# Optimization experiments

Measured on AMD Instinct MI355X. Metric: run time of the kernel, lower is better.

The kernel has to match this reference:

```python
import jax, jax.numpy as jnp
import numpy as np

N = 10000      # nodes
E = 160000     # edges
F = 64         # channels (hidden_irreps 0e multiplicity)
NS = 10        # species
NB = 8         # num_bessel
NL = 4         # max_ell + 1
LM = 16        # total SH components (l=0..3)
RMAX = 10.0
AVG = 16.0     # avg_num_neighbors
L_OF = jnp.array([0,1,1,1,2,2,2,2,2,3,3,3,3,3,3,3])  # l index of each SH component


def _sph(u):
    """Component-normalized real spherical harmonics l=0..3 on unit vectors [E,3] -> [E,16]."""
    x, y, z = u[..., 0], u[..., 1], u[..., 2]
    s3, s5, s7 = 3.0**0.5, 5.0**0.5, 7.0**0.5
    s15, s42, s70, s105 = 15.0**0.5, 42.0**0.5, 70.0**0.5, 105.0**0.5
    one = jnp.ones_like(x)
    return jnp.stack([
        one,
        s3*x, s3*y, s3*z,
        s15*x*y, s15*y*z, (s5/2)*(3*z*z - 1), s15*x*z, (s15/2)*(x*x - y*y),
        (s70/4)*y*(3*x*x - y*y), s105*x*y*z, (s42/4)*y*(5*z*z - 1),
        (s7/2)*z*(5*z*z - 3), (s42/4)*x*(5*z*z - 1),
        (s105/2)*z*(x*x - y*y), (s70/4)*x*(x*x - 3*y*y),
    ], axis=-1)


def _bessel(r):
    """Bessel radial basis with smooth polynomial cutoff. r [E] -> [E,NB]."""
    n = jnp.arange(1, NB + 1, dtype=r.dtype)
    eb = (2.0 / RMAX) ** 0.5 * jnp.sin(n * jnp.pi * r[:, None] / RMAX) / (r[:, None] + 1e-9)
    p = 5.0
    xr = r / RMAX
    env = (1.0 - ((p+1)*(p+2)/2) * xr**p + p*(p+2) * xr**(p+1) - (p*(p+1)/2) * xr**(p+2))
    env = jnp.where(xr < 1.0, env, 0.0)
    return eb * env[:, None]


def _interaction(node_feats, node_attrs, Y, bess, senders, receivers,
                 W_up, Wr1, Wr2, Wr3, W_mix, W_sc, w_prod, last):
    # linear down-projection of scalar channel feeding the edge tensor product
    h = node_feats[:, :, 0] @ W_up                                   # [N,F]
    # per-edge radial weights, one per (channel, l) path
    R = jax.nn.silu(bess @ Wr1)
    R = jax.nn.silu(R @ Wr2)
    R = (R @ Wr3).reshape(E, F, NL)                                  # [E,F,4]
    Rlm = R[:, :, L_OF]                                              # [E,F,16]
    # edge tensor-product message: gather senders, modulate by radial, outer with SH
    m = h[senders][:, :, None] * Rlm * Y[:, None, :]                 # [E,F,16]
    A = jax.ops.segment_sum(m, receivers, num_segments=N) / AVG      # [N,F,16]
    # per-l channel mixing (equivariant linear)
    A = jnp.einsum('nfk,kfg->ngk', A, W_mix[L_OF])                   # [N,F,16]
    # species-dependent residual (skip tensor product with node attrs)
    wsp = jnp.einsum('ns,sfg->nfg', node_attrs, W_sc)                # [N,F,F]
    sc = jnp.einsum('nfk,nfg->ngk', node_feats, wsp)                 # [N,F,16]
    # symmetric product basis (correlation=3): scalar-modulated polynomial, equivariant
    s = A[:, :, 0]
    B = A * (w_prod[0] + w_prod[1]*s + w_prod[2]*s*s)[:, :, None]
    out = B + sc
    if last:  # last layer keeps only 0e (scalar) irreps
        out = out * (jnp.arange(LM) == 0).astype(out.dtype)
    return out


def _forward(positions, node_attrs, shifts, senders, receivers, w_embed,
             u0_up, u0_r1, u0_r2, u0_r3, u0_mix, u0_sc, u0_prod, w_read0,
             u1_up, u1_r1, u1_r2, u1_r3, u1_mix, u1_sc, u1_prod, w_mlp1, w_mlp2):
    vec = positions[receivers] - positions[senders] + shifts         # [E,3]
    r = jnp.linalg.norm(vec, axis=-1)
    Y = _sph(vec / (r[:, None] + 1e-9))                              # [E,16]
    bess = _bessel(r)                                                # [E,8]
    # node embedding into scalar channel of [N,F,16] state
    nf = jnp.zeros((N, F, LM), positions.dtype).at[:, :, 0].set(node_attrs @ w_embed)
    nf = _interaction(nf, node_attrs, Y, bess, senders, receivers,
                      u0_up, u0_r1, u0_r2, u0_r3, u0_mix, u0_sc, u0_prod, last=False)
    out0 = nf[:, :, 0] @ w_read0                                     # [N,1] linear readout
    nf = _interaction(nf, node_attrs, Y, bess, senders, receivers,
                      u1_up, u1_r1, u1_r2, u1_r3, u1_mix, u1_sc, u1_prod, last=True)
    out1 = jax.nn.silu(nf[:, :, 0] @ w_mlp1) @ w_mlp2                # [N,1] nonlinear readout
    return jnp.stack([out0, out1], axis=1)                           # [N,2,1]


def setup_inputs() -> dict:
    key = jax.random.key(0)
    ks = jax.random.split(key, 24)
    positions = jax.random.uniform(ks[0], (N, 3), jnp.float32) * 5.0
    species = jax.random.randint(ks[1], (N,), 0, NS)
    node_attrs = jax.nn.one_hot(species, NS, dtype=jnp.float32)
    shifts = jnp.zeros((E, 3), jnp.float32)
    senders = jax.random.randint(ks[2], (E,), 0, N, dtype=jnp.int32)
    receivers = jax.random.randint(ks[3], (E,), 0, N, dtype=jnp.int32)

    def nrm(k, shape, fan_in):
        return jax.random.normal(k, shape, jnp.float32) / (fan_in ** 0.5)

    d = dict(positions=positions, node_attrs=node_attrs, shifts=shifts,
             senders=senders, receivers=receivers,
             w_embed=nrm(ks[4], (NS, F), NS))
    for i, base in ((0, 5), (1, 13)):
        d[f'u{i}_up'] = nrm(ks[base], (F, F), F)
        d[f'u{i}_r1'] = nrm(ks[base+1], (NB, 64), NB)
        d[f'u{i}_r2'] = nrm(ks[base+2], (64, 64), 64)
        d[f'u{i}_r3'] = nrm(ks[base+3], (64, F*NL), 64)
        d[f'u{i}_mix'] = nrm(ks[base+4], (NL, F, F), F)
        d[f'u{i}_sc'] = nrm(ks[base+5], (NS, F, F), F)
        d[f'u{i}_prod'] = nrm(ks[base+6], (3, F), 1)
    d['w_read0'] = nrm(ks[12], (F, 1), F)
    d['w_mlp1'] = nrm(ks[20], (F, 16), F)
    d['w_mlp2'] = nrm(ks[21], (16, 1), 16)
    return d


def reference(positions, node_attrs, shifts, senders, receivers, w_embed,
              u0_up, u0_r1, u0_r2, u0_r3, u0_mix, u0_sc, u0_prod, w_read0,
              u1_up, u1_r1, u1_r2, u1_r3, u1_mix, u1_sc, u1_prod, w_mlp1, w_mlp2):
    return _forward(positions, node_attrs, shifts, senders, receivers, w_embed,
                    u0_up, u0_r1, u0_r2, u0_r3, u0_mix, u0_sc, u0_prod, w_read0,
                    u1_up, u1_r1, u1_r2, u1_r3, u1_mix, u1_sc, u1_prod, w_mlp1, w_mlp2)
```

## Files before the change

kernel.cpp:

```cpp
#include <hip/hip_runtime.h>
#include <hip/hip_bf16.h>
#include <cstdint>
#include <cstddef>

#define NN 10000
#define NE 160000

typedef unsigned short u16;
typedef __attribute__((ext_vector_type(8))) short short8;
typedef __attribute__((ext_vector_type(4))) float f32x4;

__device__ __forceinline__ float b2f(u16 u){
    union { uint32_t i; float f; } v; v.i = ((uint32_t)u) << 16; return v.f;
}
__device__ __forceinline__ u16 f2b(float f){
    union { __hip_bfloat16 h; u16 u; } c; c.h = __float2bfloat16(f); return c.u;
}
__device__ __forceinline__ u16 f2b_rne(float f){
    uint32_t b = __float_as_uint(f);
    return (u16)((b + 0x7FFFu + ((b >> 16) & 1u)) >> 16);
}
__device__ __forceinline__ float silu_f(float x){ return x / (1.f + __expf(-x)); }
__device__ __forceinline__ float ldr(const void* p, int i, int bf){
    return bf ? b2f(((const u16*)p)[i]) : ((const float*)p)[i];
}

constexpr size_t W_FLAG = 0;
constexpr size_t W_CNT  = 16;
constexpr size_t W_OFFS = 10016;
constexpr size_t W_SSND = 30032;
constexpr size_t W_ATT  = 350032;
constexpr size_t W_WGT  = 960032;
constexpr size_t OW_EMB = 0;
constexpr size_t OW_UP0 = 640;
constexpr size_t OW_R10 = 4736;
constexpr size_t OW_R20 = 5248;
constexpr size_t OW_R30 = 9344;
constexpr size_t OW_MIX0= 25728;
constexpr size_t OW_SC0 = 42112;
constexpr size_t OW_PR0 = 83072;
constexpr size_t OW_UP1 = 83264;
constexpr size_t OW_R11 = 87360;
constexpr size_t OW_R21 = 87872;
constexpr size_t OW_R31 = 91968;
constexpr size_t OW_MIX1= 108352;
constexpr size_t OW_SC1 = 124736;
constexpr size_t OW_PR1 = 165696;
constexpr size_t OW_RD0 = 165888;
constexpr size_t OW_ML1 = 165952;
constexpr size_t OW_ML2 = 166976;
constexpr size_t OW_TEND = 167000;
constexpr size_t W_BES  = W_WGT + OW_TEND;
constexpr size_t W_NF0  = W_BES + (size_t)NE*8;
constexpr size_t W_H    = W_NF0 + (size_t)NN*64;
constexpr size_t W_A    = W_H   + (size_t)NN*64;
constexpr size_t W_NF1  = W_A   + (size_t)NN*64;
constexpr size_t W_R0   = W_NF1 + (size_t)NN*64;
constexpr size_t W_R1   = W_R0  + (size_t)NE*32;
constexpr size_t WP_DUAL   = W_R1 + (size_t)NE*32;
constexpr size_t WP_SINGLE = W_R0 + (size_t)NE*32;
constexpr size_t W_RS_F = W_R0;
constexpr size_t WP_F   = W_R0 + NE;

constexpr size_t NEED_DUAL   = (WP_DUAL   + 10400) * 4;
constexpr size_t NEED_SINGLE = (WP_SINGLE + 10400) * 4;

constexpr int OCT  = 520;
constexpr int OCTS = 136;

__global__ void k_dh(const uint32_t* __restrict__ attrs, const int* __restrict__ rcv,
                     int* __restrict__ flag, int* __restrict__ cnt, int* __restrict__ rank){
    int i = blockIdx.x * 256 + threadIdx.x;
    int c = 0;
    if (i < 50000){
        uint32_t v = attrs[i];
        c = (v != 0u && v != 0x3F800000u) ? 1 : 0;
    }
    unsigned long long m = __ballot(c);
    if ((threadIdx.x & 63) == 0 && m)
        atomicAdd(flag, (int)__popcll(m));
    if (i < NE) rank[i] = atomicAdd(&cnt[rcv[i]], 1);
}

struct PrepArgs { const void* s[21]; float* d[21]; int n[21]; };
__global__ __launch_bounds__(1024) void k_scan_prep(PrepArgs a, const int* __restrict__ flag,
        const int* __restrict__ cnt, int* __restrict__ offs,
        u16* __restrict__ WP, float* __restrict__ nf0, float* __restrict__ h){
    int bf = flag[0] > 100;
    int t = threadIdx.x;
    if (blockIdx.x == 0){
        __shared__ int cl[10000];
        __shared__ int part[1024];
        for (int i = t; i < 10000; i += 1024) cl[i] = cnt[i];
        __syncthreads();
        int base = t * 10;
        int s = 0;
        #pragma unroll
        for (int i = 0; i < 10; i++) if (base + i < NN) s += cl[base + i];
        part[t] = s; __syncthreads();
        for (int d = 1; d < 1024; d <<= 1){
            int v = part[t];
            if (t >= d) v += part[t - d];
            __syncthreads();
            part[t] = v;
            __syncthreads();
        }
        int run = part[t] - s;
        #pragma unroll
        for (int i = 0; i < 10; i++){
            int idx = base + i;
            if (idx < NN){ offs[idx] = run; run += cl[idx]; }
        }
        if (t == 1023) offs[NN] = part[1023];
    } else if (blockIdx.x < 65){
        int stride = 64 * 1024;
        int t0 = (blockIdx.x - 1) * 1024 + t;
        for (int k = 0; k < 21; k++){
            float* d = a.d[k]; int n4 = a.n[k] >> 2;
            if (bf){
                const uint2* s = (const uint2*)a.s[k];
                for (int i = t0; i < n4; i += stride){
                    uint2 v = s[i];
                    float4 o;
                    o.x = b2f((u16)(v.x & 0xffffu));
                    o.y = b2f((u16)(v.x >> 16));
                    o.z = b2f((u16)(v.y & 0xffffu));
                    o.w = b2f((u16)(v.y >> 16));
                    ((float4*)d)[i] = o;
                }
            } else {
                const float4* s = (const float4*)a.s[k];
                for (int i = t0; i < n4; i += stride) ((float4*)d)[i] = s[i];
            }
        }
    } else if (blockIdx.x < 67){
        int b = blockIdx.x - 65;
        const void* W1 = a.s[b ? 12 : 5];
        const void* W2 = a.s[b ? 13 : 6];
        const void* W3 = a.s[b ? 14 : 7];
        u16* dst = WP + b * 10400;
        for (int i = t; i < 5200; i += 1024) ((uint32_t*)dst)[i] = 0;
        __syncthreads();
        for (int i = t; i < 512; i += 1024){
            int n = i >> 3, k = i & 7;
            dst[n*8 + k] = f2b(ldr(W1, k*64 + n, bf));
        }
        for (int i = t; i < 2048; i += 1024){
            int k = (i >> 6) * 2, n = i & 63;
            uint32_t p2 = ((uint32_t)f2b(ldr(W2, (k+1)*64 + n, bf)) << 16) | f2b(ldr(W2, k*64 + n, bf));
            uint32_t p3 = ((uint32_t)f2b(ldr(W3, (k+1)*256 + 4*n, bf)) << 16) | f2b(ldr(W3, k*256 + 4*n, bf));
            *(uint32_t*)&dst[2080 + (k>>3)*OCT + n*8 + (k&7)] = p2;
            *(uint32_t*)&dst[6240 + (k>>3)*OCT + n*8 + (k&7)] = p3;
        }
    } else {
        int nb = blockIdx.x - 67;
        int n = nb*16 + (t >> 6);
        int l = t & 63;
        const void* attrs = a.s[1];
        const void* Wemb  = a.s[3];
        const void* Wup0  = a.s[4];
        float acc = 0.f;
        #pragma unroll
        for (int s = 0; s < 10; s++) acc += ldr(attrs, n*10 + s, bf) * ldr(Wemb, s*64 + l, bf);
        nf0[n*64 + l] = acc;
        float hv = 0.f;
        #pragma unroll 16
        for (int g = 0; g < 64; g++) hv += __shfl(acc, g) * ldr(Wup0, g*64 + l, bf);
        h[n*64 + l] = hv;
    }
}

__global__ void k_scatter_r(const int* __restrict__ rcv, const int* __restrict__ snd,
        const void* __restrict__ posr, const void* __restrict__ shfr,
        const int* __restrict__ offs, const int* __restrict__ rank,
        int* __restrict__ ssnd, float* __restrict__ rs,
        const int* __restrict__ flag){
    int e = blockIdx.x * 256 + threadIdx.x;
    if (e >= NE) return;
    int bf = flag[0] > 100;
    int r = rcv[e], s = snd[e];
    float vx = ldr(posr, r*3+0, bf) - ldr(posr, s*3+0, bf) + ldr(shfr, e*3+0, bf);
    float vy = ldr(posr, r*3+1, bf) - ldr(posr, s*3+1, bf) + ldr(shfr, e*3+1, bf);
    float vz = ldr(posr, r*3+2, bf) - ldr(posr, s*3+2, bf) + ldr(shfr, e*3+2, bf);
    float rr = sqrtf(vx*vx + vy*vy + vz*vz);
    int p = offs[r] + rank[e];
    ssnd[p] = s;
    rs[p] = rr;
}

__global__ void k_bess(const float* __restrict__ rs, float* __restrict__ bessp){
    int p = blockIdx.x * 256 + threadIdx.x;
    if (p >= NE) return;
    float rr = rs[p];
    float xr = rr * 0.1f;
    float x2 = xr*xr; float x5 = x2*x2*xr;
    float env = 1.f - 21.f*x5 + 35.f*x5*xr - 15.f*x5*x2;
    if (xr >= 1.f) env = 0.f;
    float scl = 0.4472135954999579f * env / (rr + 1e-9f);
    float b[8];
    #pragma unroll
    for (int n = 1; n <= 8; n++)
        b[n-1] = scl * sinf((float)n * 3.14159265358979323846f * rr * 0.1f);
    float4* be = (float4*)(bessp + (size_t)p*8);
    be[0] = make_float4(b[0], b[1], b[2], b[3]);
    be[1] = make_float4(b[4], b[5], b[6], b[7]);
}

__global__ __launch_bounds__(256) void k_mlp_mfma(
        const int* __restrict__ rcv, const int* __restrict__ snd,
        const void* __restrict__ posr, const void* __restrict__ shfr,
        const int* __restrict__ offs, const int* __restrict__ rank,
        const u16* __restrict__ WPa, const u16* __restrict__ WPb,
        int* __restrict__ ssnd, u16* __restrict__ R0, u16* __restrict__ R1,
        int nblk0, const int* __restrict__ flag){
    __shared__ __align__(16) u16 W[10400];
    __shared__ __align__(16) u16 X[4][12*OCTS];
    int bf = flag[0] > 100;
    int half = blockIdx.x >= nblk0;
    int blk  = half ? blockIdx.x - nblk0 : blockIdx.x;
    const u16* WP = half ? WPb : WPa;
    u16* R = half ? R1 : R0;
    int t = threadIdx.x;
    int w = t >> 6, lane = t & 63;
    int q = lane >> 4, r = lane & 15;
    u16* Xw = &X[w][0];
    for (int i = t; i < 1300; i += 256) ((uint4*)W)[i] = ((const uint4*)WP)[i];
    int ge = blk*256 + w*64 + lane;
    int rn = rcv[ge], sn = snd[ge];
    int pv = offs[rn] + rank[ge];
    float vx = ldr(posr, rn*3+0, bf) - ldr(posr, sn*3+0, bf) + ldr(shfr, ge*3+0, bf);
    float vy = ldr(posr, rn*3+1, bf) - ldr(posr, sn*3+1, bf) + ldr(shfr, ge*3+1, bf);
    float vz = ldr(posr, rn*3+2, bf) - ldr(posr, sn*3+2, bf) + ldr(shfr, ge*3+2, bf);
    float rre = sqrtf(vx*vx + vy*vy + vz*vz);
    if (!half) ssnd[pv] = sn;
    {
        uint32_t* xz = (uint32_t*)(Xw + OCTS);
        for (int i = lane; i < 204; i += 64) xz[i] = 0;
    }
    __syncthreads();
    #pragma unroll 1
    for (int st = 0; st < 4; st++){
        int p0 = __shfl(pv, st*16 + q*4 + 0);
        int p1 = __shfl(pv, st*16 + q*4 + 1);
        int p2 = __shfl(pv, st*16 + q*4 + 2);
        int p3 = __shfl(pv, st*16 + q*4 + 3);
        {
            float rr = __shfl(rre, st*16 + (lane >> 2));
            float xr = rr * 0.1f;
            float x2 = xr*xr, x5 = x2*x2*xr;
            float env = 1.f - 21.f*x5 + 35.f*x5*xr - 15.f*x5*x2;
            if (xr >= 1.f) env = 0.f;
            float scl = 0.4472135954999579f * env / (rr + 1e-9f);
            int k0 = (lane & 3) * 2;
            float b0 = scl * __sinf((float)(k0+1) * 0.3141592653589793f * rr);
            float b1 = scl * __sinf((float)(k0+2) * 0.3141592653589793f * rr);
            ((uint32_t*)Xw)[lane] = ((uint32_t)f2b_rne(b1) << 16) | f2b_rne(b0);
        }
        {
            short8 a = *(const short8*)&Xw[q*OCTS + r*8];
            #pragma unroll
            for (int nt = 0; nt < 4; nt++){
                short8 b = *(const short8*)&W[q*OCT + (nt*16 + r)*8];
                f32x4 c = {0.f, 0.f, 0.f, 0.f};
                c = __builtin_amdgcn_mfma_f32_16x16x32_bf16(a, b, c, 0, 0, 0);
                #pragma unroll
                for (int g = 0; g < 4; g++){
                    int e = q*4 + g;
                    int n = nt*16 + r;
                    Xw[(4 + (n>>3))*OCTS + e*8 + (n&7)] = f2b_rne(silu_f(c[g]));
                }
            }
        }
        {
            short8 a0 = *(const short8*)&Xw[(4+q)*OCTS + r*8];
            short8 a1 = *(const short8*)&Xw[(8+q)*OCTS + r*8];
            #pragma unroll
            for (int nt = 0; nt < 4; nt++){
                short8 b0 = *(const short8*)&W[2080 + q*OCT + (nt*16 + r)*8];
                short8 b1 = *(const short8*)&W[2080 + (4+q)*OCT + (nt*16 + r)*8];
                f32x4 c = {0.f, 0.f, 0.f, 0.f};
                c = __builtin_amdgcn_mfma_f32_16x16x32_bf16(a0, b0, c, 0, 0, 0);
                c = __builtin_amdgcn_mfma_f32_16x16x32_bf16(a1, b1, c, 0, 0, 0);
                #pragma unroll
                for (int g = 0; g < 4; g++){
                    int e = q*4 + g;
                    int n = nt*16 + r;
                    Xw[(4 + (n>>3))*OCTS + e*8 + (n&7)] = f2b_rne(silu_f(c[g]));
                }
            }
        }
        {
            short8 a0 = *(const short8*)&Xw[(4+q)*OCTS + r*8];
            short8 a1 = *(const short8*)&Xw[(8+q)*OCTS + r*8];
            #pragma unroll
            for (int nt = 0; nt < 4; nt++){
                short8 b0 = *(const short8*)&W[6240 + q*OCT + (nt*16 + r)*8];
                short8 b1 = *(const short8*)&W[6240 + (4+q)*OCT + (nt*16 + r)*8];
                f32x4 c = {0.f, 0.f, 0.f, 0.f};
                c = __builtin_amdgcn_mfma_f32_16x16x32_bf16(a0, b0, c, 0, 0, 0);
                c = __builtin_amdgcn_mfma_f32_16x16x32_bf16(a1, b1, c, 0, 0, 0);
                int n = nt*16 + r;
                R[(size_t)p0*64 + n] = f2b_rne(c[0]);
                R[(size_t)p1*64 + n] = f2b_rne(c[1]);
                R[(size_t)p2*64 + n] = f2b_rne(c[2]);
                R[(size_t)p3*64 + n] = f2b_rne(c[3]);
            }
        }
    }
}

template<int LAST>
__global__ __launch_bounds__(256) void k_gnode(const int* __restrict__ offs,
        const int* __restrict__ ssnd, const float* __restrict__ h, const u16* __restrict__ R,
        const float* __restrict__ nf, const float* __restrict__ attrs,
        const float* __restrict__ Wmix0, const float* __restrict__ Wsc,
        const float* __restrict__ Wprod, const float* __restrict__ Wtail,
        const float* __restrict__ Wml2, const float* __restrict__ Wup1,
        float* __restrict__ nf1out, float* __restrict__ hout,
        void* __restrict__ out, const int* __restrict__ flag){
    int wv = threadIdx.x >> 6;
    int n  = blockIdx.x * 4 + wv;
    int l  = threadIdx.x & 63;
    int beg = __builtin_amdgcn_readfirstlane(offs[n]);
    int end = __builtin_amdgcn_readfirstlane(offs[n+1]);
    float acc = 0.f;
    for (int c = beg; c < end; c += 64){
        int ld = c + l; if (ld >= end) ld = end - 1;
        int sv = ssnd[ld];
        int m = end - c; if (m > 64) m = 64;
        int j = 0;
        for (; j + 8 <= m; j += 8){
            int s0 = __builtin_amdgcn_readlane(sv, j+0);
            int s1 = __builtin_amdgcn_readlane(sv, j+1);
            int s2 = __builtin_amdgcn_readlane(sv, j+2);
            int s3 = __builtin_amdgcn_readlane(sv, j+3);
            int s4 = __builtin_amdgcn_readlane(sv, j+4);
            int s5 = __builtin_amdgcn_readlane(sv, j+5);
            int s6 = __builtin_amdgcn_readlane(sv, j+6);
            int s7 = __builtin_amdgcn_readlane(sv, j+7);
            float r0 = b2f(R[(size_t)(c+j+0)*64 + l]);
            float r1 = b2f(R[(size_t)(c+j+1)*64 + l]);
            float r2 = b2f(R[(size_t)(c+j+2)*64 + l]);
            float r3 = b2f(R[(size_t)(c+j+3)*64 + l]);
            float r4 = b2f(R[(size_t)(c+j+4)*64 + l]);
            float r5 = b2f(R[(size_t)(c+j+5)*64 + l]);
            float r6 = b2f(R[(size_t)(c+j+6)*64 + l]);
            float r7 = b2f(R[(size_t)(c+j+7)*64 + l]);
            float a0 = h[s0*64 + l]*r0 + h[s1*64 + l]*r1;
            float a1 = h[s2*64 + l]*r2 + h[s3*64 + l]*r3;
            float a2 = h[s4*64 + l]*r4 + h[s5*64 + l]*r5;
            float a3 = h[s6*64 + l]*r6 + h[s7*64 + l]*r7;
            acc += (a0 + a1) + (a2 + a3);
        }
        for (; j + 4 <= m; j += 4){
            int s0 = __builtin_amdgcn_readlane(sv, j+0);
            int s1 = __builtin_amdgcn_readlane(sv, j+1);
            int s2 = __builtin_amdgcn_readlane(sv, j+2);
            int s3 = __builtin_amdgcn_readlane(sv, j+3);
            float r0 = b2f(R[(size_t)(c+j+0)*64 + l]);
            float r1 = b2f(R[(size_t)(c+j+1)*64 + l]);
            float r2 = b2f(R[(size_t)(c+j+2)*64 + l]);
            float r3 = b2f(R[(size_t)(c+j+3)*64 + l]);
            acc += h[s0*64 + l]*r0 + h[s1*64 + l]*r1 + h[s2*64 + l]*r2 + h[s3*64 + l]*r3;
        }
        for (; j < m; j++){
            int s = __builtin_amdgcn_readlane(sv, j);
            acc += h[s*64 + l] * b2f(R[(size_t)(c+j)*64 + l]);
        }
    }
    float Af  = acc * 0.0625f;
    float nff = nf[n*64 + l];
    float am = 0.f;
    #pragma unroll 16
    for (int f = 0; f < 64; f++) am += __shfl(Af, f) * Wmix0[f*64 + l];
    float sc = 0.f;
    for (int s = 0; s < 10; s++){
        float av = attrs[n*10 + s];
        if (av != 0.f){
            const float* Ws = Wsc + s*4096;
            float t = 0.f;
            #pragma unroll 16
            for (int f = 0; f < 64; f++) t += __shfl(nff, f) * Ws[f*64 + l];
            sc += av * t;
        }
    }
    float poly = Wprod[l] + Wprod[64 + l]*am + Wprod[128 + l]*am*am;
    float val = am*poly + sc;
    float rv;
    if (LAST == 0){
        nf1out[n*64 + l] = val;
        float hv = 0.f;
        #pragma unroll 16
        for (int g = 0; g < 64; g++) hv += __shfl(val, g) * Wup1[g*64 + l];
        hout[n*64 + l] = hv;
        rv = val * Wtail[l];
    } else {
        int lj = l & 15;
        float t = 0.f;
        #pragma unroll 16
        for (int g = 0; g < 64; g++){
            float vg = __shfl(val, g);
            t += vg * Wtail[g*16 + lj];
        }
        rv = (l < 16) ? (silu_f(t) * Wml2[lj]) : 0.f;
    }
    #pragma unroll
    for (int o2 = 32; o2; o2 >>= 1) rv += __shfl_down(rv, o2);
    if (l == 0){
        int idx = 2*n + LAST;
        if (flag[0] > 100) ((__hip_bfloat16*)out)[idx] = __float2bfloat16(rv);
        else               ((float*)out)[idx] = rv;
    }
}

__global__ __launch_bounds__(256) void k_msg_fused(const int* __restrict__ offs,
        const int* __restrict__ ssnd, const float* __restrict__ h, const float* __restrict__ bessp,
        const float* __restrict__ W1, const float* __restrict__ W2, const float* __restrict__ W3,
        float* __restrict__ A){
    int wv = threadIdx.x >> 6;
    int n  = blockIdx.x * 4 + wv;
    int l  = threadIdx.x & 63;
    float w1c[8];
    #pragma unroll
    for (int i = 0; i < 8; i++) w1c[i] = W1[i*64 + l];
    float w2c[64];
    #pragma unroll
    for (int j = 0; j < 64; j++) w2c[j] = W2[j*64 + l];
    float w3c[64];
    #pragma unroll
    for (int j = 0; j < 64; j++) w3c[j] = W3[j*256 + 4*l];
    float acc = 0.f;
    int beg = __builtin_amdgcn_readfirstlane(offs[n]);
    int end = __builtin_amdgcn_readfirstlane(offs[n+1]);
    for (int p = beg; p < end; p++){
        int s = __builtin_amdgcn_readfirstlane(ssnd[p]);
        const float* be = bessp + (size_t)p*8;
        float h1 = 0.f;
        #pragma unroll
        for (int i = 0; i < 8; i++) h1 += be[i] * w1c[i];
        h1 = silu_f(h1);
        float h2 = 0.f;
        #pragma unroll
        for (int j = 0; j < 64; j++) h2 += __shfl(h1, j) * w2c[j];
        h2 = silu_f(h2);
        float rr = 0.f;
        #pragma unroll
        for (int j = 0; j < 64; j++) rr += __shfl(h2, j) * w3c[j];
        acc += h[s*64 + l] * rr;
    }
    A[n*64 + l] = acc * 0.0625f;
}
template<int LAST>
__global__ __launch_bounds__(256) void k_node(const float* __restrict__ A, const float* __restrict__ nf,
        const float* __restrict__ attrs, const float* __restrict__ Wmix0, const float* __restrict__ Wsc,
        const float* __restrict__ Wprod, const float* __restrict__ Wtail, const float* __restrict__ Wml2,
        const float* __restrict__ Wup1, float* __restrict__ nf1out, float* __restrict__ hout,
        void* __restrict__ out, const int* __restrict__ flag){
    int wv = threadIdx.x >> 6;
    int n  = blockIdx.x * 4 + wv;
    int l  = threadIdx.x & 63;
    float Af  = A[n*64 + l];
    float nff = nf[n*64 + l];
    float am = 0.f;
    #pragma unroll 16
    for (int f = 0; f < 64; f++) am += __shfl(Af, f) * Wmix0[f*64 + l];
    float sc = 0.f;
    for (int s = 0; s < 10; s++){
        float av = attrs[n*10 + s];
        if (av != 0.f){
            const float* Ws = Wsc + s*4096;
            float t = 0.f;
            #pragma unroll 16
            for (int f = 0; f < 64; f++) t += __shfl(nff, f) * Ws[f*64 + l];
            sc += av * t;
        }
    }
    float poly = Wprod[l] + Wprod[64 + l]*am + Wprod[128 + l]*am*am;
    float val = am*poly + sc;
    float rv;
    if (LAST == 0){
        nf1out[n*64 + l] = val;
        float hv = 0.f;
        #pragma unroll 16
        for (int g = 0; g < 64; g++) hv += __shfl(val, g) * Wup1[g*64 + l];
        hout[n*64 + l] = hv;
        rv = val * Wtail[l];
    } else {
        int lj = l & 15;
        float t = 0.f;
        #pragma unroll 16
        for (int g = 0; g < 64; g++){
            float vg = __shfl(val, g);
            t += vg * Wtail[g*16 + lj];
        }
        rv = (l < 16) ? (silu_f(t) * Wml2[lj]) : 0.f;
    }
    #pragma unroll
    for (int o2 = 32; o2; o2 >>= 1) rv += __shfl_down(rv, o2);
    if (l == 0){
        int idx = 2*n + LAST;
        if (flag[0] > 100) ((__hip_bfloat16*)out)[idx] = __float2bfloat16(rv);
        else               ((float*)out)[idx] = rv;
    }
}

extern "C" void kernel_launch(void* const* d_in, const int* in_sizes, int n_in,
                              void* d_out, int out_size, void* d_ws, size_t ws_size,
                              hipStream_t stream) {
    int*   iw = (int*)d_ws;
    float* fw = (float*)d_ws;
    const int* snd = (const int*)d_in[3];
    const int* rcv = (const int*)d_in[4];

    PrepArgs pa;
    const int    pidx[21] = {0,1,2, 5,6,7,8,9,10,11,12,13,14,15,16,17,18,19,20,21,22};
    const size_t pdst[21] = {W_ATT, W_ATT, W_ATT,
        W_WGT+OW_EMB, W_WGT+OW_UP0, W_WGT+OW_R10, W_WGT+OW_R20, W_WGT+OW_R30,
        W_WGT+OW_MIX0, W_WGT+OW_SC0, W_WGT+OW_PR0,
        W_WGT+OW_UP1, W_WGT+OW_R11, W_WGT+OW_R21, W_WGT+OW_R31,
        W_WGT+OW_MIX1, W_WGT+OW_SC1, W_WGT+OW_PR1,
        W_WGT+OW_RD0, W_WGT+OW_ML1, W_WGT+OW_ML2};
    const int    pn[21]   = {0, 100000, 0,
        640, 4096, 512, 4096, 16384, 16384, 40960, 192,
        4096, 512, 4096, 16384, 16384, 40960, 192, 64, 1024, 16};
    for (int i = 0; i < 21; i++){
        pa.s[i] = d_in[pidx[i]];
        pa.d[i] = fw + pdst[i];
        pa.n[i] = pn[i];
    }

    const int dual   = (ws_size >= NEED_DUAL);
    const int single = (!dual && ws_size >= NEED_SINGLE);
    const size_t wp  = dual ? WP_DUAL : (single ? WP_SINGLE : WP_F);
    int* rank = iw + W_BES;

    hipMemsetAsync(iw, 0, (W_CNT + NN) * sizeof(int), stream);
    k_dh<<<NE/256, 256, 0, stream>>>((const uint32_t*)d_in[1], rcv, iw + W_FLAG, iw + W_CNT, rank);
    k_scan_prep<<<692, 1024, 0, stream>>>(pa, iw + W_FLAG, iw + W_CNT, iw + W_OFFS,
                                          (u16*)(fw + wp), fw + W_NF0, fw + W_H);

    if (dual){
        k_mlp_mfma<<<1250, 256, 0, stream>>>(rcv, snd, d_in[0], d_in[2],
                                             iw + W_OFFS, rank,
                                             (const u16*)(fw + wp), (const u16*)(fw + wp) + 10400,
                                             iw + W_SSND, (u16*)(fw + W_R0), (u16*)(fw + W_R1),
                                             625, iw + W_FLAG);
        k_gnode<0><<<NN/4, 256, 0, stream>>>(iw+W_OFFS, iw+W_SSND, fw+W_H, (const u16*)(fw+W_R0),
            fw+W_NF0, fw+W_ATT, fw+W_WGT+OW_MIX0, fw+W_WGT+OW_SC0, fw+W_WGT+OW_PR0,
            fw+W_WGT+OW_RD0, nullptr, fw+W_WGT+OW_UP1, fw+W_NF1, fw+W_A, d_out, iw+W_FLAG);
        k_gnode<1><<<NN/4, 256, 0, stream>>>(iw+W_OFFS, iw+W_SSND, fw+W_A, (const u16*)(fw+W_R1),
            fw+W_NF1, fw+W_ATT, fw+W_WGT+OW_MIX1, fw+W_WGT+OW_SC1, fw+W_WGT+OW_PR1,
            fw+W_WGT+OW_ML1, fw+W_WGT+OW_ML2, nullptr, nullptr, nullptr, d_out, iw+W_FLAG);
    } else if (single){
        k_mlp_mfma<<<625, 256, 0, stream>>>(rcv, snd, d_in[0], d_in[2],
                                            iw + W_OFFS, rank,
                                            (const u16*)(fw + wp), (const u16*)(fw + wp),
                                            iw + W_SSND, (u16*)(fw + W_R0), (u16*)(fw + W_R0),
                                            2000000, iw + W_FLAG);
        k_gnode<0><<<NN/4, 256, 0, stream>>>(iw+W_OFFS, iw+W_SSND, fw+W_H, (const u16*)(fw+W_R0),
            fw+W_NF0, fw+W_ATT, fw+W_WGT+OW_MIX0, fw+W_WGT+OW_SC0, fw+W_WGT+OW_PR0,
            fw+W_WGT+OW_RD0, nullptr, fw+W_WGT+OW_UP1, fw+W_NF1, fw+W_A, d_out, iw+W_FLAG);
        k_mlp_mfma<<<625, 256, 0, stream>>>(rcv, snd, d_in[0], d_in[2],
                                            iw + W_OFFS, rank,
                                            (const u16*)(fw + wp) + 10400, (const u16*)(fw + wp) + 10400,
                                            iw + W_SSND, (u16*)(fw + W_R0), (u16*)(fw + W_R0),
                                            2000000, iw + W_FLAG);
        k_gnode<1><<<NN/4, 256, 0, stream>>>(iw+W_OFFS, iw+W_SSND, fw+W_A, (const u16*)(fw+W_R0),
            fw+W_NF1, fw+W_ATT, fw+W_WGT+OW_MIX1, fw+W_WGT+OW_SC1, fw+W_WGT+OW_PR1,
            fw+W_WGT+OW_ML1, fw+W_WGT+OW_ML2, nullptr, nullptr, nullptr, d_out, iw+W_FLAG);
    } else {
        k_scatter_r<<<NE/256, 256, 0, stream>>>(rcv, snd, d_in[0], d_in[2],
                                                iw + W_OFFS, rank, iw + W_SSND,
                                                fw + W_RS_F, iw + W_FLAG);
        k_bess<<<NE/256, 256, 0, stream>>>(fw + W_RS_F, fw + W_BES);
        k_msg_fused<<<NN/4, 256, 0, stream>>>(iw+W_OFFS, iw+W_SSND, fw+W_H, fw+W_BES,
                                              fw+W_WGT+OW_R10, fw+W_WGT+OW_R20,
                                              fw+W_WGT+OW_R30, fw + W_A);
        k_node<0><<<NN/4, 256, 0, stream>>>(fw + W_A, fw + W_NF0, fw + W_ATT,
                                            fw + W_WGT + OW_MIX0, fw + W_WGT + OW_SC0,
                                            fw + W_WGT + OW_PR0, fw + W_WGT + OW_RD0, nullptr,
                                            fw + W_WGT + OW_UP1, fw + W_NF1, fw + W_H,
                                            d_out, iw + W_FLAG);
        k_msg_fused<<<NN/4, 256, 0, stream>>>(iw+W_OFFS, iw+W_SSND, fw+W_H, fw+W_BES,
                                              fw+W_WGT+OW_R11, fw+W_WGT+OW_R21,
                                              fw+W_WGT+OW_R31, fw + W_A);
        k_node<1><<<NN/4, 256, 0, stream>>>(fw + W_A, fw + W_NF1, fw + W_ATT,
                                            fw + W_WGT + OW_MIX1, fw + W_WGT + OW_SC1,
                                            fw + W_WGT + OW_PR1, fw + W_WGT + OW_ML1,
                                            fw + W_WGT + OW_ML2, nullptr, nullptr, nullptr,
                                            d_out, iw + W_FLAG);
    }
}
```

Before: 215.1 us.

## Fuse layer-1 radial MLP into layer-0 gather kernel as extra blocks

```diff
diff --git a/kernel.cpp b/kernel.cpp
--- a/kernel.cpp
+++ b/kernel.cpp
@@ -206,25 +206,14 @@
     be[1] = make_float4(b[4], b[5], b[6], b[7]);
 }
 
-__global__ __launch_bounds__(256) void k_mlp_mfma(
+template<int WRITE_SSND>
+__device__ __forceinline__ void mlp_body(int blk,
         const int* __restrict__ rcv, const int* __restrict__ snd,
         const void* __restrict__ posr, const void* __restrict__ shfr,
         const int* __restrict__ offs, const int* __restrict__ rank,
-        const u16* __restrict__ WPa, const u16* __restrict__ WPb,
-        int* __restrict__ ssnd, u16* __restrict__ R0, u16* __restrict__ R1,
-        int nblk0, const int* __restrict__ flag){
-    __shared__ __align__(16) u16 W[10400];
-    __shared__ __align__(16) u16 X[4][12*OCTS];
-    int bf = flag[0] > 100;
-    int half = blockIdx.x >= nblk0;
-    int blk  = half ? blockIdx.x - nblk0 : blockIdx.x;
-    const u16* WP = half ? WPb : WPa;
-    u16* R = half ? R1 : R0;
-    int t = threadIdx.x;
-    int w = t >> 6, lane = t & 63;
+        const u16* __restrict__ W, int* __restrict__ ssnd, u16* __restrict__ R,
+        u16* Xw, int bf, int w, int lane){
     int q = lane >> 4, r = lane & 15;
-    u16* Xw = &X[w][0];
-    for (int i = t; i < 1300; i += 256) ((uint4*)W)[i] = ((const uint4*)WP)[i];
     int ge = blk*256 + w*64 + lane;
     int rn = rcv[ge], sn = snd[ge];
     int pv = offs[rn] + rank[ge];
@@ -232,7 +221,7 @@
     float vy = ldr(posr, rn*3+1, bf) - ldr(posr, sn*3+1, bf) + ldr(shfr, ge*3+1, bf);
     float vz = ldr(posr, rn*3+2, bf) - ldr(posr, sn*3+2, bf) + ldr(shfr, ge*3+2, bf);
     float rre = sqrtf(vx*vx + vy*vy + vz*vz);
-    if (!half) ssnd[pv] = sn;
+    if (WRITE_SSND) ssnd[pv] = sn;
     {
         uint32_t* xz = (uint32_t*)(Xw + OCTS);
         for (int i = lane; i < 204; i += 64) xz[i] = 0;
@@ -309,18 +298,33 @@
     }
 }
 
+__global__ __launch_bounds__(256) void k_mlp_mfma(
+        const int* __restrict__ rcv, const int* __restrict__ snd,
+        const void* __restrict__ posr, const void* __restrict__ shfr,
+        const int* __restrict__ offs, const int* __restrict__ rank,
+        const u16* __restrict__ WP,
+        int* __restrict__ ssnd, u16* __restrict__ R,
+        const int* __restrict__ flag){
+    __shared__ __align__(16) u16 W[10400];
+    __shared__ __align__(16) u16 X[4][12*OCTS];
+    int bf = flag[0] > 100;
+    int t = threadIdx.x;
+    int w = t >> 6, lane = t & 63;
+    for (int i = t; i < 1300; i += 256) ((uint4*)W)[i] = ((const uint4*)WP)[i];
+    mlp_body<1>(blockIdx.x, rcv, snd, posr, shfr, offs, rank, W, ssnd, R,
+                &X[w][0], bf, w, lane);
+}
+
 template<int LAST>
-__global__ __launch_bounds__(256) void k_gnode(const int* __restrict__ offs,
-        const int* __restrict__ ssnd, const float* __restrict__ h, const u16* __restrict__ R,
+__device__ __forceinline__ void gnode_body(int n, int l,
+        const int* __restrict__ offs, const int* __restrict__ ssnd,
+        const float* __restrict__ h, const u16* __restrict__ R,
         const float* __restrict__ nf, const float* __restrict__ attrs,
         const float* __restrict__ Wmix0, const float* __restrict__ Wsc,
         const float* __restrict__ Wprod, const float* __restrict__ Wtail,
         const float* __restrict__ Wml2, const float* __restrict__ Wup1,
         float* __restrict__ nf1out, float* __restrict__ hout,
         void* __restrict__ out, const int* __restrict__ flag){
-    int wv = threadIdx.x >> 6;
-    int n  = blockIdx.x * 4 + wv;
-    int l  = threadIdx.x & 63;
     int beg = __builtin_amdgcn_readfirstlane(offs[n]);
     int end = __builtin_amdgcn_readfirstlane(offs[n+1]);
     float acc = 0.f;
@@ -410,6 +414,49 @@
         int idx = 2*n + LAST;
         if (flag[0] > 100) ((__hip_bfloat16*)out)[idx] = __float2bfloat16(rv);
         else               ((float*)out)[idx] = rv;
+    }
+}
+
+template<int LAST>
+__global__ __launch_bounds__(256) void k_gnode(const int* __restrict__ offs,
+        const int* __restrict__ ssnd, const float* __restrict__ h, const u16* __restrict__ R,
+        const float* __restrict__ nf, const float* __restrict__ attrs,
+        const float* __restrict__ Wmix0, const float* __restrict__ Wsc,
+        const float* __restrict__ Wprod, const float* __restrict__ Wtail,
+        const float* __restrict__ Wml2, const float* __restrict__ Wup1,
+        float* __restrict__ nf1out, float* __restrict__ hout,
+        void* __restrict__ out, const int* __restrict__ flag){
+    int n = blockIdx.x * 4 + (threadIdx.x >> 6);
+    int l = threadIdx.x & 63;
+    gnode_body<LAST>(n, l, offs, ssnd, h, R, nf, attrs, Wmix0, Wsc, Wprod,
+                     Wtail, Wml2, Wup1, nf1out, hout, out, flag);
+}
+
+__global__ __launch_bounds__(256) void k_gnode0_mlp1(
+        const int* __restrict__ offs, const int* __restrict__ ssnd,
+        const float* __restrict__ h, const u16* __restrict__ R0,
+        const float* __restrict__ nf, const float* __restrict__ attrs,
+        const float* __restrict__ Wmix0, const float* __restrict__ Wsc,
+        const float* __restrict__ Wprod, const float* __restrict__ Wtail,
+        const float* __restrict__ Wup1,
+        float* __restrict__ nf1out, float* __restrict__ hout,
+        void* __restrict__ out,
+        const int* __restrict__ rcv, const int* __restrict__ snd,
+        const void* __restrict__ posr, const void* __restrict__ shfr,
+        const int* __restrict__ rank, const u16* __restrict__ WP1,
+        u16* __restrict__ R1,
+        const int* __restrict__ flag){
+    __shared__ __align__(16) u16 X[4][12*OCTS];
+    int t = threadIdx.x;
+    int w = t >> 6, lane = t & 63;
+    if (blockIdx.x < 2500){
+        int n = blockIdx.x * 4 + w;
+        gnode_body<0>(n, lane, offs, ssnd, h, R0, nf, attrs, Wmix0, Wsc, Wprod,
+                      Wtail, nullptr, Wup1, nf1out, hout, out, flag);
+    } else {
+        int bf = flag[0] > 100;
+        mlp_body<0>(blockIdx.x - 2500, rcv, snd, posr, shfr, offs, rank,
+                    WP1, nullptr, R1, &X[w][0], bf, w, lane);
     }
 }
 
@@ -540,31 +587,31 @@
                                           (u16*)(fw + wp), fw + W_NF0, fw + W_H);
 
     if (dual){
-        k_mlp_mfma<<<1250, 256, 0, stream>>>(rcv, snd, d_in[0], d_in[2],
-                                             iw + W_OFFS, rank,
-                                             (const u16*)(fw + wp), (const u16*)(fw + wp) + 10400,
-                                             iw + W_SSND, (u16*)(fw + W_R0), (u16*)(fw + W_R1),
-                                             625, iw + W_FLAG);
-        k_gnode<0><<<NN/4, 256, 0, stream>>>(iw+W_OFFS, iw+W_SSND, fw+W_H, (const u16*)(fw+W_R0),
+        k_mlp_mfma<<<625, 256, 0, stream>>>(rcv, snd, d_in[0], d_in[2],
+                                            iw + W_OFFS, rank,
+                                            (const u16*)(fw + wp),
+                                            iw + W_SSND, (u16*)(fw + W_R0), iw + W_FLAG);
+        k_gnode0_mlp1<<<3125, 256, 0, stream>>>(
+            iw+W_OFFS, iw+W_SSND, fw+W_H, (const u16*)(fw+W_R0),
             fw+W_NF0, fw+W_ATT, fw+W_WGT+OW_MIX0, fw+W_WGT+OW_SC0, fw+W_WGT+OW_PR0,
-            fw+W_WGT+OW_RD0, nullptr, fw+W_WGT+OW_UP1, fw+W_NF1, fw+W_A, d_out, iw+W_FLAG);
+            fw+W_WGT+OW_RD0, fw+W_WGT+OW_UP1, fw+W_NF1, fw+W_A, d_out,
+            rcv, snd, d_in[0], d_in[2], rank, (const u16*)(fw + wp) + 10400,
+            (u16*)(fw + W_R1), iw+W_FLAG);
         k_gnode<1><<<NN/4, 256, 0, stream>>>(iw+W_OFFS, iw+W_SSND, fw+W_A, (const u16*)(fw+W_R1),
             fw+W_NF1, fw+W_ATT, fw+W_WGT+OW_MIX1, fw+W_WGT+OW_SC1, fw+W_WGT+OW_PR1,
             fw+W_WGT+OW_ML1, fw+W_WGT+OW_ML2, nullptr, nullptr, nullptr, d_out, iw+W_FLAG);
     } else if (single){
         k_mlp_mfma<<<625, 256, 0, stream>>>(rcv, snd, d_in[0], d_in[2],
                                             iw + W_OFFS, rank,
-                                            (const u16*)(fw + wp), (const u16*)(fw + wp),
-                                            iw + W_SSND, (u16*)(fw + W_R0), (u16*)(fw + W_R0),
-                                            2000000, iw + W_FLAG);
+                                            (const u16*)(fw + wp),
+                                            iw + W_SSND, (u16*)(fw + W_R0), iw + W_FLAG);
         k_gnode<0><<<NN/4, 256, 0, stream>>>(iw+W_OFFS, iw+W_SSND, fw+W_H, (const u16*)(fw+W_R0),
             fw+W_NF0, fw+W_ATT, fw+W_WGT+OW_MIX0, fw+W_WGT+OW_SC0, fw+W_WGT+OW_PR0,
             fw+W_WGT+OW_RD0, nullptr, fw+W_WGT+OW_UP1, fw+W_NF1, fw+W_A, d_out, iw+W_FLAG);
         k_mlp_mfma<<<625, 256, 0, stream>>>(rcv, snd, d_in[0], d_in[2],
                                             iw + W_OFFS, rank,
-                                            (const u16*)(fw + wp) + 10400, (const u16*)(fw + wp) + 10400,
-                                            iw + W_SSND, (u16*)(fw + W_R0), (u16*)(fw + W_R0),
-                                            2000000, iw + W_FLAG);
+                                            (const u16*)(fw + wp) + 10400,
+                                            iw + W_SSND, (u16*)(fw + W_R0), iw + W_FLAG);
         k_gnode<1><<<NN/4, 256, 0, stream>>>(iw+W_OFFS, iw+W_SSND, fw+W_A, (const u16*)(fw+W_R0),
             fw+W_NF1, fw+W_ATT, fw+W_WGT+OW_MIX1, fw+W_WGT+OW_SC1, fw+W_WGT+OW_PR1,
             fw+W_WGT+OW_ML1, fw+W_WGT+OW_ML2, nullptr, nullptr, nullptr, d_out, iw+W_FLAG);
```

Result: slower. 232.7 us (+8.2%).
